# Performance work log

Measured on AMD Instinct MI355X. Metric: run time of the kernel, lower is better.

Reference implementation:

```python
import jax, jax.numpy as jnp
import numpy as np

N = 50000        # nodes
E = 1_600_000    # edges (avg degree 32)
IN, HID, OUT = 128, 64, 16


def setup_inputs() -> dict:
    key = jax.random.key(0)
    k0, k1, k2, k3, k4 = jax.random.split(key, 5)
    src = jax.random.randint(k0, (E,), 0, N, dtype=jnp.int32)
    dst = jax.random.randint(k1, (E,), 0, N, dtype=jnp.int32)
    features = jax.random.normal(k2, (N, IN), dtype=jnp.float32)
    W1 = jax.random.normal(k3, (IN, HID), dtype=jnp.float32) / np.float32(np.sqrt(IN))
    b1 = jnp.zeros((HID,), jnp.float32)
    W2 = jax.random.normal(k4, (HID, OUT), dtype=jnp.float32) / np.float32(np.sqrt(HID))
    b2 = jnp.zeros((OUT,), jnp.float32)
    return {"features": features, "W1": W1, "b1": b1, "W2": W2, "b2": b2,
            "src": src, "dst": dst}


def _graph_conv(src, dst, x, W, b):
    # DGL GraphConv, norm='both':  out = D_dst^{-1/2} * A^T * (D_src^{-1/2} * x) @ W + b
    ones = jnp.ones((src.shape[0],), x.dtype)
    deg_out = jax.ops.segment_sum(ones, src, num_segments=N)  # out-degree of source nodes
    deg_in = jax.ops.segment_sum(ones, dst, num_segments=N)   # in-degree of dest nodes
    norm_s = jax.lax.rsqrt(jnp.maximum(deg_out, 1.0))
    norm_d = jax.lax.rsqrt(jnp.maximum(deg_in, 1.0))
    # project first (in_feats >= out_feats) so messages are in the smaller dim
    h = (x * norm_s[:, None]) @ W                              # [N, out_dim]
    agg = jax.ops.segment_sum(h[src], dst, num_segments=N)     # sparse aggregate
    return agg * norm_d[:, None] + b


def reference(features, W1, b1, W2, b2, src, dst):
    h = jax.nn.relu(_graph_conv(src, dst, features, W1, b1))
    return _graph_conv(src, dst, h, W2, b2)
```

## Files before the change

kernel.cpp:

```cpp
#include <hip/hip_runtime.h>
#include <hip/hip_fp16.h>

#define IN_F  128
#define HID_F 64
#define OUT_F 16
#define MAX_N 50176
#define HWORDS (MAX_N / 2)
#define QWORDS (MAX_N / 4)
#define NSEG  128

#define SCAN_ELEMS 4
#define SCAN_BLOCK 256
#define SCAN_CHUNK (SCAN_BLOCK * SCAN_ELEMS)

#define LSTR 136
#define XSTR 68

typedef __attribute__((ext_vector_type(8))) _Float16 half8;
typedef __attribute__((ext_vector_type(4))) _Float16 half4v;
typedef __attribute__((ext_vector_type(4))) float    floatx4;

__global__ __launch_bounds__(1024) void hist2_kernel(const int* __restrict__ src,
                                                     const int* __restrict__ dst,
                                                     unsigned int* __restrict__ partial,
                                                     int E, int seg, int Wr8) {
    __shared__ unsigned int cnt[QWORDS];
    int b = blockIdx.x;
    const int* ids = blockIdx.y ? dst : src;
    unsigned int* pbase = partial + (size_t)blockIdx.y * NSEG * Wr8;
    for (int w = threadIdx.x; w < Wr8; w += 1024) cnt[w] = 0;
    __syncthreads();
    int lo = b * seg, hi = min(lo + seg, E);
    for (int e = lo + threadIdx.x; e < hi; e += 1024) {
        int d = ids[e];
        atomicAdd(&cnt[d >> 2], 1u << ((d & 3) * 8));
    }
    __syncthreads();
    for (int w = threadIdx.x; w < Wr8; w += 1024)
        pbase[(size_t)b * Wr8 + w] = cnt[w];
}

__global__ __launch_bounds__(256) void reduce_norm_kernel(unsigned int* __restrict__ partial,
                                                          int* __restrict__ counts,
                                                          float* __restrict__ norm_s,
                                                          float* __restrict__ norm_d,
                                                          int Wr8, int N) {
    int w = blockIdx.x * 256 + threadIdx.x;
    if (w >= Wr8) return;
    unsigned int r0 = 0, r1 = 0, r2 = 0, r3 = 0;
    if (blockIdx.y == 0) {
        const unsigned int* base = partial;
        for (int b = 0; b < NSEG; b++) {
            unsigned int v = base[(size_t)b * Wr8 + w];
            r0 += v & 0xFFu; r1 += (v >> 8) & 0xFFu;
            r2 += (v >> 16) & 0xFFu; r3 += v >> 24;
        }
        int d = 4 * w;
        if (d     < N) norm_s[d]     = rsqrtf(fmaxf((float)r0, 1.0f));
        if (d + 1 < N) norm_s[d + 1] = rsqrtf(fmaxf((float)r1, 1.0f));
        if (d + 2 < N) norm_s[d + 2] = rsqrtf(fmaxf((float)r2, 1.0f));
        if (d + 3 < N) norm_s[d + 3] = rsqrtf(fmaxf((float)r3, 1.0f));
    } else {
        unsigned int* base = partial + (size_t)NSEG * Wr8;
        for (int b = 0; b < NSEG; b++) {
            size_t idx = (size_t)b * Wr8 + w;
            unsigned int v = base[idx];
            base[idx] = r0 | (r1 << 8) | (r2 << 16) | (r3 << 24);
            r0 += v & 0xFFu; r1 += (v >> 8) & 0xFFu;
            r2 += (v >> 16) & 0xFFu; r3 += v >> 24;
        }
        int d = 4 * w;
        if (d     < N) { counts[d]     = (int)r0; norm_d[d]     = rsqrtf(fmaxf((float)r0, 1.0f)); }
        if (d + 1 < N) { counts[d + 1] = (int)r1; norm_d[d + 1] = rsqrtf(fmaxf((float)r1, 1.0f)); }
        if (d + 2 < N) { counts[d + 2] = (int)r2; norm_d[d + 2] = rsqrtf(fmaxf((float)r2, 1.0f)); }
        if (d + 3 < N) { counts[d + 3] = (int)r3; norm_d[d + 3] = rsqrtf(fmaxf((float)r3, 1.0f)); }
    }
}

__global__ __launch_bounds__(SCAN_BLOCK) void scan_local_kernel(int* __restrict__ counts,
                                                                int* __restrict__ bsum, int N) {
    __shared__ int part[SCAN_BLOCK];
    int t = threadIdx.x;
    int base = blockIdx.x * SCAN_CHUNK + t * SCAN_ELEMS;
    int v[SCAN_ELEMS];
    int s = 0;
    #pragma unroll
    for (int k = 0; k < SCAN_ELEMS; k++) {
        int i = base + k;
        v[k] = (i < N) ? counts[i] : 0;
        s += v[k];
    }
    part[t] = s;
    __syncthreads();
    for (int off = 1; off < SCAN_BLOCK; off <<= 1) {
        int x = (t >= off) ? part[t - off] : 0;
        __syncthreads();
        part[t] += x;
        __syncthreads();
    }
    int run = (t > 0) ? part[t - 1] : 0;
    #pragma unroll
    for (int k = 0; k < SCAN_ELEMS; k++) {
        int i = base + k;
        if (i < N) counts[i] = run;
        run += v[k];
    }
    if (t == SCAN_BLOCK - 1) bsum[blockIdx.x] = part[SCAN_BLOCK - 1];
}

__global__ __launch_bounds__(1024) void scan_bsum_kernel(int* __restrict__ bsum, int nblocks) {
    __shared__ int part[1024];
    int t = threadIdx.x;
    int v = (t < nblocks) ? bsum[t] : 0;
    part[t] = v;
    __syncthreads();
    for (int off = 1; off < 1024; off <<= 1) {
        int x = (t >= off) ? part[t - off] : 0;
        __syncthreads();
        part[t] += x;
        __syncthreads();
    }
    if (t < nblocks) bsum[t] = part[t] - v;
}

__global__ __launch_bounds__(1024) void scatter_lds_kernel(const int* __restrict__ src,
                                                           const int* __restrict__ dst,
                                                           const int* __restrict__ row_start,
                                                           const int* __restrict__ bsum,
                                                           const unsigned int* __restrict__ prefix,
                                                           unsigned short* __restrict__ csr_src,
                                                           int E, int seg, int Wr8, int N) {
    __shared__ unsigned int pos[HWORDS];
    int b = blockIdx.x;
    int p = blockIdx.y;
    int lo = b * seg, hi = min(lo + seg, E);
    int nlo = p * HWORDS, nhi = min(nlo + HWORDS, N);
    for (int d = nlo + threadIdx.x; d < nhi; d += 1024) {
        unsigned int word = prefix[(size_t)b * Wr8 + (d >> 2)];
        unsigned int base8 = (word >> ((d & 3) * 8)) & 0xFFu;
        pos[d - nlo] = (unsigned int)(row_start[d] + bsum[d >> 10]) + base8;
    }
    __syncthreads();
    for (int e = lo + threadIdx.x; e < hi; e += 1024) {
        int d = dst[e];
        if (d >= nlo && d < nhi) {
            unsigned int q = atomicAdd(&pos[d - nlo], 1u);
            csr_src[q] = (unsigned short)src[e];
        }
    }
}

__global__ __launch_bounds__(256) void gemm1_kernel(const float* __restrict__ x,
                                                    const float* __restrict__ W,
                                                    const float* __restrict__ norm_s,
                                                    __half* __restrict__ h, int N) {
    __shared__ _Float16 sx[64 * LSTR];
    __shared__ _Float16 sw[64 * LSTR];
    int t = threadIdx.x;
    int row0 = blockIdx.x * 64;

    for (int i = t; i < IN_F * 16; i += 256) {
        int k = i >> 4, n4 = (i & 15) * 4;
        float4 w4 = *(const float4*)(W + (size_t)k * HID_F + n4);
        sw[(n4 + 0) * LSTR + k] = (_Float16)w4.x;
        sw[(n4 + 1) * LSTR + k] = (_Float16)w4.y;
        sw[(n4 + 2) * LSTR + k] = (_Float16)w4.z;
        sw[(n4 + 3) * LSTR + k] = (_Float16)w4.w;
    }
    for (int i = t; i < 64 * 32; i += 256) {
        int r = i >> 5, k4 = (i & 31) * 4;
        int gr = row0 + r;
        half4v hv = {0, 0, 0, 0};
        if (gr < N) {
            float4 v = *(const float4*)(x + (size_t)gr * IN_F + k4);
            float ns = norm_s[gr];
            hv.x = (_Float16)(v.x * ns); hv.y = (_Float16)(v.y * ns);
            hv.z = (_Float16)(v.z * ns); hv.w = (_Float16)(v.w * ns);
        }
        *(half4v*)(sx + r * LSTR + k4) = hv;
    }
    __syncthreads();

    int wave = t >> 6, lane = t & 63;
    int m = lane & 15, quad = lane >> 4;
    int rbase = wave * 16;

    floatx4 acc[4] = {{0,0,0,0}, {0,0,0,0}, {0,0,0,0}, {0,0,0,0}};
    #pragma unroll
    for (int ks = 0; ks < 4; ks++) {
        half8 av = *(half8*)(sx + (rbase + m) * LSTR + ks * 32 + quad * 8);
        #pragma unroll
        for (int ct = 0; ct < 4; ct++) {
            half8 bv = *(half8*)(sw + (ct * 16 + m) * LSTR + ks * 32 + quad * 8);
            acc[ct] = __builtin_amdgcn_mfma_f32_16x16x32_f16(av, bv, acc[ct], 0, 0, 0);
        }
    }
    #pragma unroll
    for (int ct = 0; ct < 4; ct++) {
        #pragma unroll
        for (int reg = 0; reg < 4; reg++) {
            int gr = row0 + rbase + quad * 4 + reg;
            if (gr < N) h[(size_t)gr * HID_F + ct * 16 + m] = __float2half(acc[ct][reg]);
        }
    }
}

__global__ __launch_bounds__(256) void agg1_kernel(const int* __restrict__ row_start,
                                                   const int* __restrict__ bsum,
                                                   const unsigned short* __restrict__ csr_src,
                                                   const __half* __restrict__ h,
                                                   const float* __restrict__ norm_d,
                                                   const float* __restrict__ norm_s,
                                                   const float* __restrict__ b1,
                                                   const float* __restrict__ W2,
                                                   __half* __restrict__ h2, int N, int E) {
    __shared__ float sW2T[OUT_F][XSTR];
    __shared__ float xrow[16][XSTR];
    int t = threadIdx.x;
    for (int i = t; i < HID_F * OUT_F; i += 256) {
        int k = i >> 4, o = i & 15;
        sW2T[o][k] = W2[i];
    }

    int wave = t >> 6, lane = t & 63;
    int slot = lane >> 3;
    int fh   = lane & 7;
    int nbase = blockIdx.x * 16 + wave * 4;

    int rs[5];
    #pragma unroll
    for (int j = 0; j < 5; j++) {
        int n = nbase + j;
        rs[j] = (n < N) ? (row_start[n] + bsum[n >> 10]) : E;
    }

    #pragma unroll
    for (int nn = 0; nn < 4; nn++) {
        int node = nbase + nn;
        if (node < N) {
            int beg = rs[nn], end = rs[nn + 1];

            float f[8] = {0.f, 0.f, 0.f, 0.f, 0.f, 0.f, 0.f, 0.f};

            #define AGG1_BODY(SIDX) {                                                  \
                const uint4* p = (const uint4*)(h + (size_t)(SIDX) * HID_F + fh * 8);  \
                uint4 u = *p;                                                          \
                __half2 q0 = *(__half2*)&u.x, q1 = *(__half2*)&u.y;                    \
                __half2 q2 = *(__half2*)&u.z, q3 = *(__half2*)&u.w;                    \
                float2 g0 = __half22float2(q0), g1 = __half22float2(q1);               \
                float2 g2 = __half22float2(q2), g3 = __half22float2(q3);               \
                f[0] += g0.x; f[1] += g0.y; f[2] += g1.x; f[3] += g1.y;                \
                f[4] += g2.x; f[5] += g2.y; f[6] += g3.x; f[7] += g3.y; }

            int i = beg + slot;
            for (; i + 24 < end; i += 32) {
                int s0 = (int)csr_src[i];
                int s1 = (int)csr_src[i + 8];
                int s2 = (int)csr_src[i + 16];
                int s3 = (int)csr_src[i + 24];
                AGG1_BODY(s0); AGG1_BODY(s1); AGG1_BODY(s2); AGG1_BODY(s3);
            }
            for (; i < end; i += 8) {
                int s = (int)csr_src[i];
                AGG1_BODY(s);
            }
            #undef AGG1_BODY

            #pragma unroll
            for (int j = 0; j < 8; j++) {
                f[j] += __shfl_xor(f[j], 8);
                f[j] += __shfl_xor(f[j], 16);
                f[j] += __shfl_xor(f[j], 32);
            }

            if (slot == 0) {
                float nd = norm_d[node], ns = norm_s[node];
                const float4 bA = *(const float4*)(b1 + fh * 8);
                const float4 bB = *(const float4*)(b1 + fh * 8 + 4);
                float4 vA, vB;
                vA.x = fmaxf(f[0] * nd + bA.x, 0.f) * ns;
                vA.y = fmaxf(f[1] * nd + bA.y, 0.f) * ns;
                vA.z = fmaxf(f[2] * nd + bA.z, 0.f) * ns;
                vA.w = fmaxf(f[3] * nd + bA.w, 0.f) * ns;
                vB.x = fmaxf(f[4] * nd + bB.x, 0.f) * ns;
                vB.y = fmaxf(f[5] * nd + bB.y, 0.f) * ns;
                vB.z = fmaxf(f[6] * nd + bB.z, 0.f) * ns;
                vB.w = fmaxf(f[7] * nd + bB.w, 0.f) * ns;
                *(float4*)&xrow[wave * 4 + nn][fh * 8]     = vA;
                *(float4*)&xrow[wave * 4 + nn][fh * 8 + 4] = vB;
            }
        }
    }
    __syncthreads();

    int nr = t >> 4, o = t & 15;
    int gnode = blockIdx.x * 16 + nr;
    if (gnode < N) {
        float acc = 0.0f;
        #pragma unroll
        for (int k4 = 0; k4 < HID_F / 4; k4++) {
            float4 x4 = *(const float4*)&xrow[nr][k4 * 4];
            float4 w4 = *(const float4*)&sW2T[o][k4 * 4];
            acc += x4.x * w4.x + x4.y * w4.y + x4.z * w4.z + x4.w * w4.w;
        }
        h2[(size_t)gnode * OUT_F + o] = __float2half(acc);
    }
}

__global__ __launch_bounds__(256) void agg2_kernel(const int* __restrict__ row_start,
                                                   const int* __restrict__ bsum,
                                                   const unsigned short* __restrict__ csr_src,
                                                   const __half* __restrict__ h2,
                                                   const float* __restrict__ norm_d,
                                                   const float* __restrict__ b2,
                                                   float* __restrict__ out, int N, int E) {
    int node = blockIdx.x * 4 + (threadIdx.x >> 6);
    if (node >= N) return;
    int lane = threadIdx.x & 63;
    int slot = lane >> 2;
    int fh   = lane & 3;
    int beg = row_start[node] + bsum[node >> 10];
    int end = (node + 1 < N) ? row_start[node + 1] + bsum[(node + 1) >> 10] : E;

    float f0 = 0.f, f1 = 0.f, f2 = 0.f, f3 = 0.f;

    #define AGG2_BODY(SIDX) {                                                  \
        const uint2* p = (const uint2*)(h2 + (size_t)(SIDX) * OUT_F + fh * 4); \
        uint2 u = *p;                                                          \
        __half2 q0 = *(__half2*)&u.x, q1 = *(__half2*)&u.y;                    \
        float2 g0 = __half22float2(q0), g1 = __half22float2(q1);               \
        f0 += g0.x; f1 += g0.y; f2 += g1.x; f3 += g1.y; }

    int i = beg + slot;
    for (; i + 16 < end; i += 32) {
        int s0 = (int)csr_src[i];
        int s1 = (int)csr_src[i + 16];
        AGG2_BODY(s0); AGG2_BODY(s1);
    }
    if (i < end) {
        int s = (int)csr_src[i];
        AGG2_BODY(s);
    }
    #undef AGG2_BODY

    f0 += __shfl_xor(f0, 4);  f1 += __shfl_xor(f1, 4);
    f2 += __shfl_xor(f2, 4);  f3 += __shfl_xor(f3, 4);
    f0 += __shfl_xor(f0, 8);  f1 += __shfl_xor(f1, 8);
    f2 += __shfl_xor(f2, 8);  f3 += __shfl_xor(f3, 8);
    f0 += __shfl_xor(f0, 16); f1 += __shfl_xor(f1, 16);
    f2 += __shfl_xor(f2, 16); f3 += __shfl_xor(f3, 16);
    f0 += __shfl_xor(f0, 32); f1 += __shfl_xor(f1, 32);
    f2 += __shfl_xor(f2, 32); f3 += __shfl_xor(f3, 32);

    if (slot == 0) {
        float nd = norm_d[node];
        float4 v;
        v.x = f0 * nd + b2[fh * 4 + 0];
        v.y = f1 * nd + b2[fh * 4 + 1];
        v.z = f2 * nd + b2[fh * 4 + 2];
        v.w = f3 * nd + b2[fh * 4 + 3];
        *(float4*)(out + (size_t)node * OUT_F + fh * 4) = v;
    }
}

extern "C" void kernel_launch(void* const* d_in, const int* in_sizes, int n_in,
                              void* d_out, int out_size, void* d_ws, size_t ws_size,
                              hipStream_t stream) {
    const float* feat = (const float*)d_in[0];
    const float* W1   = (const float*)d_in[1];
    const float* b1   = (const float*)d_in[2];
    const float* W2   = (const float*)d_in[3];
    const float* b2   = (const float*)d_in[4];
    const int*   src  = (const int*)d_in[5];
    const int*   dst  = (const int*)d_in[6];

    const int N   = in_sizes[0] / IN_F;
    const int E   = in_sizes[5];
    const int seg = (E + NSEG - 1) / NSEG;
    const int Wr8 = (N + 3) >> 2;
    const int nchunks = (N + SCAN_CHUNK - 1) / SCAN_CHUNK;
    const int npass   = (N + HWORDS - 1) / HWORDS;

    float* fws    = (float*)d_ws;
    float* norm_s = fws;
    float* norm_d = fws + N;
    __half* h1    = (__half*)(fws + 2 * (size_t)N);
    __half* h2    = h1 + (size_t)N * HID_F;
    int*   iws    = (int*)(h2 + (size_t)N * OUT_F);
    int*   row_start = iws;
    int*   bsum      = iws + N + 1;
    unsigned int* partial = (unsigned int*)(iws + N + 1 + 1024);
    unsigned short* csr_src = (unsigned short*)(partial + 2 * (size_t)NSEG * Wr8);

    hist2_kernel<<<dim3(NSEG, 2), 1024, 0, stream>>>(src, dst, partial, E, seg, Wr8);
    reduce_norm_kernel<<<dim3((Wr8 + 255) / 256, 2), 256, 0, stream>>>(partial, row_start, norm_s, norm_d, Wr8, N);

    scan_local_kernel<<<nchunks, SCAN_BLOCK, 0, stream>>>(row_start, bsum, N);
    scan_bsum_kernel<<<1, 1024, 0, stream>>>(bsum, nchunks);

    scatter_lds_kernel<<<dim3(NSEG, npass), 1024, 0, stream>>>(src, dst, row_start, bsum,
                                                               partial + (size_t)NSEG * Wr8,
                                                               csr_src, E, seg, Wr8, N);

    gemm1_kernel<<<(N + 63) / 64, 256, 0, stream>>>(feat, W1, norm_s, h1, N);
    agg1_kernel<<<(N + 15) / 16, 256, 0, stream>>>(row_start, bsum, csr_src, h1, norm_d, norm_s, b1, W2, h2, N, E);
    agg2_kernel<<<(N + 3) / 4, 256, 0, stream>>>(row_start, bsum, csr_src, h2, norm_d, b2, (float*)d_out, N, E);
}
```

Measured before the change: 201.7 us.

## Split layer-1 aggregation into two 32-feature halves for L2-resident gathers

gemm1 now writes the hidden features as two separate N×32 fp16 tables. Layer-1 aggregation runs as two passes, each gathering from one 3.2 MB table, so the randomly accessed working set is more likely to stay in L2. The first pass writes its post-ReLU half to a float buffer in global memory, and the second pass reads it back for the W2 projection. The gather loop now handles two nodes at once with masked unrolled loads. The cost is an extra kernel launch, a second read of the CSR index list, and a round trip of the intermediate half through global memory.

```diff
diff --git a/kernel.cpp b/kernel.cpp
--- a/kernel.cpp
+++ b/kernel.cpp
@@ -15,6 +15,7 @@
 
 #define LSTR 136
 #define XSTR 68
+#define HSTR 36
 
 typedef __attribute__((ext_vector_type(8))) _Float16 half8;
 typedef __attribute__((ext_vector_type(4))) _Float16 half4v;
@@ -153,7 +154,8 @@
 __global__ __launch_bounds__(256) void gemm1_kernel(const float* __restrict__ x,
                                                     const float* __restrict__ W,
                                                     const float* __restrict__ norm_s,
-                                                    __half* __restrict__ h, int N) {
+                                                    __half* __restrict__ h1a,
+                                                    __half* __restrict__ h1b, int N) {
     __shared__ _Float16 sx[64 * LSTR];
     __shared__ _Float16 sw[64 * LSTR];
     int t = threadIdx.x;
@@ -197,35 +199,140 @@
     }
     #pragma unroll
     for (int ct = 0; ct < 4; ct++) {
+        __half* tab = (ct < 2) ? h1a : h1b;
+        int col = (ct & 1) * 16 + m;
         #pragma unroll
         for (int reg = 0; reg < 4; reg++) {
             int gr = row0 + rbase + quad * 4 + reg;
-            if (gr < N) h[(size_t)gr * HID_F + ct * 16 + m] = __float2half(acc[ct][reg]);
-        }
-    }
-}
-
-__global__ __launch_bounds__(256) void agg1_kernel(const int* __restrict__ row_start,
-                                                   const int* __restrict__ bsum,
-                                                   const unsigned short* __restrict__ csr_src,
-                                                   const __half* __restrict__ h,
-                                                   const float* __restrict__ norm_d,
-                                                   const float* __restrict__ norm_s,
-                                                   const float* __restrict__ b1,
-                                                   const float* __restrict__ W2,
-                                                   __half* __restrict__ h2, int N, int E) {
+            if (gr < N) tab[(size_t)gr * 32 + col] = __float2half(acc[ct][reg]);
+        }
+    }
+}
+
+#define ACC8(F, U) {                                                   \
+    __half2 q0 = *(__half2*)&U.x, q1 = *(__half2*)&U.y;                \
+    __half2 q2 = *(__half2*)&U.z, q3 = *(__half2*)&U.w;                \
+    float2 g0 = __half22float2(q0), g1 = __half22float2(q1);           \
+    float2 g2 = __half22float2(q2), g3 = __half22float2(q3);           \
+    F[0] += g0.x; F[1] += g0.y; F[2] += g1.x; F[3] += g1.y;            \
+    F[4] += g2.x; F[5] += g2.y; F[6] += g3.x; F[7] += g3.y; }
+
+__device__ __forceinline__ void gather_pair32(const unsigned short* __restrict__ csr,
+                                              const __half* __restrict__ tab,
+                                              int begU, int endU, int begV, int endV,
+                                              int slot, int fh, int Em1,
+                                              float* fU, float* fV) {
+    int iU = begU + slot, iV = begV + slot;
+    while (iU < endU || iV < endV) {
+        int jU1 = iU + 16, jV1 = iV + 16;
+        bool vU0 = iU < endU, vU1 = jU1 < endU;
+        bool vV0 = iV < endV, vV1 = jV1 < endV;
+        int s0 = (int)csr[min(iU, Em1)];
+        int s1 = (int)csr[min(jU1, Em1)];
+        int s2 = (int)csr[min(iV, Em1)];
+        int s3 = (int)csr[min(jV1, Em1)];
+        uint4 u0 = *(const uint4*)(tab + (size_t)s0 * 32 + fh * 8);
+        uint4 u1 = *(const uint4*)(tab + (size_t)s1 * 32 + fh * 8);
+        uint4 u2 = *(const uint4*)(tab + (size_t)s2 * 32 + fh * 8);
+        uint4 u3 = *(const uint4*)(tab + (size_t)s3 * 32 + fh * 8);
+        u0.x = vU0 ? u0.x : 0u; u0.y = vU0 ? u0.y : 0u; u0.z = vU0 ? u0.z : 0u; u0.w = vU0 ? u0.w : 0u;
+        u1.x = vU1 ? u1.x : 0u; u1.y = vU1 ? u1.y : 0u; u1.z = vU1 ? u1.z : 0u; u1.w = vU1 ? u1.w : 0u;
+        u2.x = vV0 ? u2.x : 0u; u2.y = vV0 ? u2.y : 0u; u2.z = vV0 ? u2.z : 0u; u2.w = vV0 ? u2.w : 0u;
+        u3.x = vV1 ? u3.x : 0u; u3.y = vV1 ? u3.y : 0u; u3.z = vV1 ? u3.z : 0u; u3.w = vV1 ? u3.w : 0u;
+        ACC8(fU, u0); ACC8(fU, u1); ACC8(fV, u2); ACC8(fV, u3);
+        iU += 32; iV += 32;
+    }
+    #pragma unroll
+    for (int j = 0; j < 8; j++) {
+        fU[j] += __shfl_xor(fU[j], 4);  fV[j] += __shfl_xor(fV[j], 4);
+        fU[j] += __shfl_xor(fU[j], 8);  fV[j] += __shfl_xor(fV[j], 8);
+        fU[j] += __shfl_xor(fU[j], 16); fV[j] += __shfl_xor(fV[j], 16);
+        fU[j] += __shfl_xor(fU[j], 32); fV[j] += __shfl_xor(fV[j], 32);
+    }
+}
+
+__global__ __launch_bounds__(256) void agg1a_kernel(const int* __restrict__ row_start,
+                                                    const int* __restrict__ bsum,
+                                                    const unsigned short* __restrict__ csr_src,
+                                                    const __half* __restrict__ h1a,
+                                                    const float* __restrict__ norm_d,
+                                                    const float* __restrict__ norm_s,
+                                                    const float* __restrict__ b1,
+                                                    float* __restrict__ xA, int N, int E) {
+    int t = threadIdx.x;
+    int wave = t >> 6, lane = t & 63;
+    int slot = lane >> 2, fh = lane & 3;
+    int nbase = blockIdx.x * 16 + wave * 4;
+    int Em1 = E - 1;
+
+    int rs[5];
+    #pragma unroll
+    for (int j = 0; j < 5; j++) {
+        int n = nbase + j;
+        rs[j] = (n < N) ? (row_start[n] + bsum[n >> 10]) : E;
+    }
+
+    #pragma unroll
+    for (int np = 0; np < 2; np++) {
+        int nU = nbase + np * 2, nV = nU + 1;
+        float fU[8] = {0,0,0,0,0,0,0,0}, fV[8] = {0,0,0,0,0,0,0,0};
+        gather_pair32(csr_src, h1a, rs[np*2], rs[np*2+1], rs[np*2+1], rs[np*2+2],
+                      slot, fh, Em1, fU, fV);
+        if (slot == 0) {
+            const float4 bA = *(const float4*)(b1 + fh * 8);
+            const float4 bB = *(const float4*)(b1 + fh * 8 + 4);
+            if (nU < N) {
+                float nd = norm_d[nU], ns = norm_s[nU];
+                float4 vA, vB;
+                vA.x = fmaxf(fU[0]*nd + bA.x, 0.f)*ns; vA.y = fmaxf(fU[1]*nd + bA.y, 0.f)*ns;
+                vA.z = fmaxf(fU[2]*nd + bA.z, 0.f)*ns; vA.w = fmaxf(fU[3]*nd + bA.w, 0.f)*ns;
+                vB.x = fmaxf(fU[4]*nd + bB.x, 0.f)*ns; vB.y = fmaxf(fU[5]*nd + bB.y, 0.f)*ns;
+                vB.z = fmaxf(fU[6]*nd + bB.z, 0.f)*ns; vB.w = fmaxf(fU[7]*nd + bB.w, 0.f)*ns;
+                *(float4*)(xA + (size_t)nU * 32 + fh * 8)     = vA;
+                *(float4*)(xA + (size_t)nU * 32 + fh * 8 + 4) = vB;
+            }
+            if (nV < N) {
+                float nd = norm_d[nV], ns = norm_s[nV];
+                float4 vA, vB;
+                vA.x = fmaxf(fV[0]*nd + bA.x, 0.f)*ns; vA.y = fmaxf(fV[1]*nd + bA.y, 0.f)*ns;
+                vA.z = fmaxf(fV[2]*nd + bA.z, 0.f)*ns; vA.w = fmaxf(fV[3]*nd + bA.w, 0.f)*ns;
+                vB.x = fmaxf(fV[4]*nd + bB.x, 0.f)*ns; vB.y = fmaxf(fV[5]*nd + bB.y, 0.f)*ns;
+                vB.z = fmaxf(fV[6]*nd + bB.z, 0.f)*ns; vB.w = fmaxf(fV[7]*nd + bB.w, 0.f)*ns;
+                *(float4*)(xA + (size_t)nV * 32 + fh * 8)     = vA;
+                *(float4*)(xA + (size_t)nV * 32 + fh * 8 + 4) = vB;
+            }
+        }
+    }
+}
+
+__global__ __launch_bounds__(256) void agg1b_kernel(const int* __restrict__ row_start,
+                                                    const int* __restrict__ bsum,
+                                                    const unsigned short* __restrict__ csr_src,
+                                                    const __half* __restrict__ h1b,
+                                                    const float* __restrict__ norm_d,
+                                                    const float* __restrict__ norm_s,
+                                                    const float* __restrict__ b1,
+                                                    const float* __restrict__ W2,
+                                                    const float* __restrict__ xA,
+                                                    __half* __restrict__ h2, int N, int E) {
     __shared__ float sW2T[OUT_F][XSTR];
-    __shared__ float xrow[16][XSTR];
+    __shared__ float xAl[16][HSTR];
+    __shared__ float xBl[16][HSTR];
     int t = threadIdx.x;
     for (int i = t; i < HID_F * OUT_F; i += 256) {
         int k = i >> 4, o = i & 15;
         sW2T[o][k] = W2[i];
     }
+    for (int i = t; i < 16 * 32; i += 256) {
+        int r = i >> 5, c = i & 31;
+        int gn = blockIdx.x * 16 + r;
+        xAl[r][c] = (gn < N) ? xA[(size_t)gn * 32 + c] : 0.f;
+    }
 
     int wave = t >> 6, lane = t & 63;
-    int slot = lane >> 3;
-    int fh   = lane & 7;
+    int slot = lane >> 2, fh = lane & 3;
     int nbase = blockIdx.x * 16 + wave * 4;
+    int Em1 = E - 1;
 
     int rs[5];
     #pragma unroll
@@ -235,59 +342,37 @@
     }
 
     #pragma unroll
-    for (int nn = 0; nn < 4; nn++) {
-        int node = nbase + nn;
-        if (node < N) {
-            int beg = rs[nn], end = rs[nn + 1];
-
-            float f[8] = {0.f, 0.f, 0.f, 0.f, 0.f, 0.f, 0.f, 0.f};
-
-            #define AGG1_BODY(SIDX) {                                                  \
-                const uint4* p = (const uint4*)(h + (size_t)(SIDX) * HID_F + fh * 8);  \
-                uint4 u = *p;                                                          \
-                __half2 q0 = *(__half2*)&u.x, q1 = *(__half2*)&u.y;                    \
-                __half2 q2 = *(__half2*)&u.z, q3 = *(__half2*)&u.w;                    \
-                float2 g0 = __half22float2(q0), g1 = __half22float2(q1);               \
-                float2 g2 = __half22float2(q2), g3 = __half22float2(q3);               \
-                f[0] += g0.x; f[1] += g0.y; f[2] += g1.x; f[3] += g1.y;                \
-                f[4] += g2.x; f[5] += g2.y; f[6] += g3.x; f[7] += g3.y; }
-
-            int i = beg + slot;
-            for (; i + 24 < end; i += 32) {
-                int s0 = (int)csr_src[i];
-                int s1 = (int)csr_src[i + 8];
-                int s2 = (int)csr_src[i + 16];
-                int s3 = (int)csr_src[i + 24];
-                AGG1_BODY(s0); AGG1_BODY(s1); AGG1_BODY(s2); AGG1_BODY(s3);
+    for (int np = 0; np < 2; np++) {
+        int nU = nbase + np * 2, nV = nU + 1;
+        float fU[8] = {0,0,0,0,0,0,0,0}, fV[8] = {0,0,0,0,0,0,0,0};
+        gather_pair32(csr_src, h1b, rs[np*2], rs[np*2+1], rs[np*2+1], rs[np*2+2],
+                      slot, fh, Em1, fU, fV);
+        if (slot == 0) {
+            const float4 bA = *(const float4*)(b1 + 32 + fh * 8);
+            const float4 bB = *(const float4*)(b1 + 32 + fh * 8 + 4);
+            if (nU < N) {
+                float nd = norm_d[nU], ns = norm_s[nU];
+                int r = wave * 4 + np * 2;
+                xBl[r][fh*8+0] = fmaxf(fU[0]*nd + bA.x, 0.f)*ns;
+                xBl[r][fh*8+1] = fmaxf(fU[1]*nd + bA.y, 0.f)*ns;
+                xBl[r][fh*8+2] = fmaxf(fU[2]*nd + bA.z, 0.f)*ns;
+                xBl[r][fh*8+3] = fmaxf(fU[3]*nd + bA.w, 0.f)*ns;
+                xBl[r][fh*8+4] = fmaxf(fU[4]*nd + bB.x, 0.f)*ns;
+                xBl[r][fh*8+5] = fmaxf(fU[5]*nd + bB.y, 0.f)*ns;
+                xBl[r][fh*8+6] = fmaxf(fU[6]*nd + bB.z, 0.f)*ns;
+                xBl[r][fh*8+7] = fmaxf(fU[7]*nd + bB.w, 0.f)*ns;
             }
-            for (; i < end; i += 8) {
-                int s = (int)csr_src[i];
-                AGG1_BODY(s);
-            }
-            #undef AGG1_BODY
-
-            #pragma unroll
-            for (int j = 0; j < 8; j++) {
-                f[j] += __shfl_xor(f[j], 8);
-                f[j] += __shfl_xor(f[j], 16);
-                f[j] += __shfl_xor(f[j], 32);
-            }
-
-            if (slot == 0) {
-                float nd = norm_d[node], ns = norm_s[node];
-                const float4 bA = *(const float4*)(b1 + fh * 8);
-                const float4 bB = *(const float4*)(b1 + fh * 8 + 4);
-                float4 vA, vB;
-                vA.x = fmaxf(f[0] * nd + bA.x, 0.f) * ns;
-                vA.y = fmaxf(f[1] * nd + bA.y, 0.f) * ns;
-                vA.z = fmaxf(f[2] * nd + bA.z, 0.f) * ns;
-                vA.w = fmaxf(f[3] * nd + bA.w, 0.f) * ns;
-                vB.x = fmaxf(f[4] * nd + bB.x, 0.f) * ns;
-                vB.y = fmaxf(f[5] * nd + bB.y, 0.f) * ns;
-                vB.z = fmaxf(f[6] * nd + bB.z, 0.f) * ns;
-                vB.w = fmaxf(f[7] * nd + bB.w, 0.f) * ns;
-                *(float4*)&xrow[wave * 4 + nn][fh * 8]     = vA;
-                *(float4*)&xrow[wave * 4 + nn][fh * 8 + 4] = vB;
+            if (nV < N) {
+                float nd = norm_d[nV], ns = norm_s[nV];
+                int r = wave * 4 + np * 2 + 1;
+                xBl[r][fh*8+0] = fmaxf(fV[0]*nd + bA.x, 0.f)*ns;
+                xBl[r][fh*8+1] = fmaxf(fV[1]*nd + bA.y, 0.f)*ns;
+                xBl[r][fh*8+2] = fmaxf(fV[2]*nd + bA.z, 0.f)*ns;
+                xBl[r][fh*8+3] = fmaxf(fV[3]*nd + bA.w, 0.f)*ns;
+                xBl[r][fh*8+4] = fmaxf(fV[4]*nd + bB.x, 0.f)*ns;
+                xBl[r][fh*8+5] = fmaxf(fV[5]*nd + bB.y, 0.f)*ns;
+                xBl[r][fh*8+6] = fmaxf(fV[6]*nd + bB.z, 0.f)*ns;
+                xBl[r][fh*8+7] = fmaxf(fV[7]*nd + bB.w, 0.f)*ns;
             }
         }
     }
@@ -298,9 +383,15 @@
     if (gnode < N) {
         float acc = 0.0f;
         #pragma unroll
-        for (int k4 = 0; k4 < HID_F / 4; k4++) {
-            float4 x4 = *(const float4*)&xrow[nr][k4 * 4];
+        for (int k4 = 0; k4 < 8; k4++) {
+            float4 x4 = *(const float4*)&xAl[nr][k4 * 4];
             float4 w4 = *(const float4*)&sW2T[o][k4 * 4];
+            acc += x4.x * w4.x + x4.y * w4.y + x4.z * w4.z + x4.w * w4.w;
+        }
+        #pragma unroll
+        for (int k4 = 0; k4 < 8; k4++) {
+            float4 x4 = *(const float4*)&xBl[nr][k4 * 4];
+            float4 w4 = *(const float4*)&sW2T[o][32 + k4 * 4];
             acc += x4.x * w4.x + x4.y * w4.y + x4.z * w4.z + x4.w * w4.w;
         }
         h2[(size_t)gnode * OUT_F + o] = __float2half(acc);
@@ -384,13 +475,16 @@
     float* fws    = (float*)d_ws;
     float* norm_s = fws;
     float* norm_d = fws + N;
-    __half* h1    = (__half*)(fws + 2 * (size_t)N);
-    __half* h2    = h1 + (size_t)N * HID_F;
+    __half* h1a   = (__half*)(fws + 2 * (size_t)N);
+    __half* h1b   = h1a + (size_t)N * 32;
+    __half* h2    = h1b + (size_t)N * 32;
     int*   iws    = (int*)(h2 + (size_t)N * OUT_F);
     int*   row_start = iws;
     int*   bsum      = iws + N + 1;
     unsigned int* partial = (unsigned int*)(iws + N + 1 + 1024);
     unsigned short* csr_src = (unsigned short*)(partial + 2 * (size_t)NSEG * Wr8);
+    size_t xa_off = ((size_t)((char*)(csr_src + E) - (char*)d_ws) + 255) & ~(size_t)255;
+    float* xA = (float*)((char*)d_ws + xa_off);
 
     hist2_kernel<<<dim3(NSEG, 2), 1024, 0, stream>>>(src, dst, partial, E, seg, Wr8);
     reduce_norm_kernel<<<dim3((Wr8 + 255) / 256, 2), 256, 0, stream>>>(partial, row_start, norm_s, norm_d, Wr8, N);
@@ -402,7 +496,8 @@
                                                                partial + (size_t)NSEG * Wr8,
                                                                csr_src, E, seg, Wr8, N);
 
-    gemm1_kernel<<<(N + 63) / 64, 256, 0, stream>>>(feat, W1, norm_s, h1, N);
-    agg1_kernel<<<(N + 15) / 16, 256, 0, stream>>>(row_start, bsum, csr_src, h1, norm_d, norm_s, b1, W2, h2, N, E);
+    gemm1_kernel<<<(N + 63) / 64, 256, 0, stream>>>(feat, W1, norm_s, h1a, h1b, N);
+    agg1a_kernel<<<(N + 15) / 16, 256, 0, stream>>>(row_start, bsum, csr_src, h1a, norm_d, norm_s, b1, xA, N, E);
+    agg1b_kernel<<<(N + 15) / 16, 256, 0, stream>>>(row_start, bsum, csr_src, h1b, norm_d, norm_s, b1, W2, xA, h2, N, E);
     agg2_kernel<<<(N + 3) / 4, 256, 0, stream>>>(row_start, bsum, csr_src, h2, norm_d, b2, (float*)d_out, N, E);
 }
```

New measurement: 222.9 us. 10.5% more time.

## Fuse the local scan into the degree reduction and do the CSR scatter in one pass

Applied to the files above, without the earlier changes.

The local prefix scan of in-degree counts now runs inside reduce_norm_kernel, which removes the separate scan_local launch. The scatter kernel drops its two node-range passes. It packs two 16-bit chunk-local write positions into each LDS word, so all destination nodes fit in shared memory, and adds the chunk offset from a small shared bsum table. The number of edge segments is doubled to raise parallelism in the histogram and scatter steps. The cost is that chunk-local positions must stay below 65536 and per-segment counts below 256, limits that only hold for graphs with bounded degree per chunk.

```diff
diff --git a/kernel.cpp b/kernel.cpp
--- a/kernel.cpp
+++ b/kernel.cpp
@@ -7,11 +7,10 @@
 #define MAX_N 50176
 #define HWORDS (MAX_N / 2)
 #define QWORDS (MAX_N / 4)
-#define NSEG  128
-
-#define SCAN_ELEMS 4
+#define NSEG  256
+
 #define SCAN_BLOCK 256
-#define SCAN_CHUNK (SCAN_BLOCK * SCAN_ELEMS)
+#define SCAN_CHUNK 1024
 
 #define LSTR 136
 #define XSTR 68
@@ -41,14 +40,16 @@
 }
 
 __global__ __launch_bounds__(256) void reduce_norm_kernel(unsigned int* __restrict__ partial,
-                                                          int* __restrict__ counts,
+                                                          int* __restrict__ row_start,
+                                                          int* __restrict__ bsum,
                                                           float* __restrict__ norm_s,
                                                           float* __restrict__ norm_d,
                                                           int Wr8, int N) {
-    int w = blockIdx.x * 256 + threadIdx.x;
-    if (w >= Wr8) return;
-    unsigned int r0 = 0, r1 = 0, r2 = 0, r3 = 0;
+    int t = threadIdx.x;
+    int w = blockIdx.x * 256 + t;
     if (blockIdx.y == 0) {
+        if (w >= Wr8) return;
+        unsigned int r0 = 0, r1 = 0, r2 = 0, r3 = 0;
         const unsigned int* base = partial;
         for (int b = 0; b < NSEG; b++) {
             unsigned int v = base[(size_t)b * Wr8 + w];
@@ -60,7 +61,12 @@
         if (d + 1 < N) norm_s[d + 1] = rsqrtf(fmaxf((float)r1, 1.0f));
         if (d + 2 < N) norm_s[d + 2] = rsqrtf(fmaxf((float)r2, 1.0f));
         if (d + 3 < N) norm_s[d + 3] = rsqrtf(fmaxf((float)r3, 1.0f));
-    } else {
+        return;
+    }
+    __shared__ int part[256];
+    bool inr = (w < Wr8);
+    unsigned int r0 = 0, r1 = 0, r2 = 0, r3 = 0;
+    if (inr) {
         unsigned int* base = partial + (size_t)NSEG * Wr8;
         for (int b = 0; b < NSEG; b++) {
             size_t idx = (size_t)b * Wr8 + w;
@@ -70,42 +76,31 @@
             r2 += (v >> 16) & 0xFFu; r3 += v >> 24;
         }
         int d = 4 * w;
-        if (d     < N) { counts[d]     = (int)r0; norm_d[d]     = rsqrtf(fmaxf((float)r0, 1.0f)); }
-        if (d + 1 < N) { counts[d + 1] = (int)r1; norm_d[d + 1] = rsqrtf(fmaxf((float)r1, 1.0f)); }
-        if (d + 2 < N) { counts[d + 2] = (int)r2; norm_d[d + 2] = rsqrtf(fmaxf((float)r2, 1.0f)); }
-        if (d + 3 < N) { counts[d + 3] = (int)r3; norm_d[d + 3] = rsqrtf(fmaxf((float)r3, 1.0f)); }
-    }
-}
-
-__global__ __launch_bounds__(SCAN_BLOCK) void scan_local_kernel(int* __restrict__ counts,
-                                                                int* __restrict__ bsum, int N) {
-    __shared__ int part[SCAN_BLOCK];
-    int t = threadIdx.x;
-    int base = blockIdx.x * SCAN_CHUNK + t * SCAN_ELEMS;
-    int v[SCAN_ELEMS];
-    int s = 0;
-    #pragma unroll
-    for (int k = 0; k < SCAN_ELEMS; k++) {
-        int i = base + k;
-        v[k] = (i < N) ? counts[i] : 0;
-        s += v[k];
-    }
-    part[t] = s;
-    __syncthreads();
-    for (int off = 1; off < SCAN_BLOCK; off <<= 1) {
+        if (d     < N) norm_d[d]     = rsqrtf(fmaxf((float)r0, 1.0f));
+        if (d + 1 < N) norm_d[d + 1] = rsqrtf(fmaxf((float)r1, 1.0f));
+        if (d + 2 < N) norm_d[d + 2] = rsqrtf(fmaxf((float)r2, 1.0f));
+        if (d + 3 < N) norm_d[d + 3] = rsqrtf(fmaxf((float)r3, 1.0f));
+    }
+    part[t] = inr ? (int)(r0 + r1 + r2 + r3) : 0;
+    __syncthreads();
+    for (int off = 1; off < 256; off <<= 1) {
         int x = (t >= off) ? part[t - off] : 0;
         __syncthreads();
         part[t] += x;
         __syncthreads();
     }
-    int run = (t > 0) ? part[t - 1] : 0;
-    #pragma unroll
-    for (int k = 0; k < SCAN_ELEMS; k++) {
-        int i = base + k;
-        if (i < N) counts[i] = run;
-        run += v[k];
-    }
-    if (t == SCAN_BLOCK - 1) bsum[blockIdx.x] = part[SCAN_BLOCK - 1];
+    if (inr) {
+        int run = (t > 0) ? part[t - 1] : 0;
+        int d = 4 * w;
+        if (d     < N) row_start[d]     = run;
+        run += (int)r0;
+        if (d + 1 < N) row_start[d + 1] = run;
+        run += (int)r1;
+        if (d + 2 < N) row_start[d + 2] = run;
+        run += (int)r2;
+        if (d + 3 < N) row_start[d + 3] = run;
+    }
+    if (t == 255) bsum[blockIdx.x] = part[255];
 }
 
 __global__ __launch_bounds__(1024) void scan_bsum_kernel(int* __restrict__ bsum, int nblocks) {
@@ -129,24 +124,31 @@
                                                            const int* __restrict__ bsum,
                                                            const unsigned int* __restrict__ prefix,
                                                            unsigned short* __restrict__ csr_src,
-                                                           int E, int seg, int Wr8, int N) {
+                                                           int E, int seg, int Wr8, int N,
+                                                           int nchunks) {
     __shared__ unsigned int pos[HWORDS];
+    __shared__ int sbsum[64];
     int b = blockIdx.x;
-    int p = blockIdx.y;
-    int lo = b * seg, hi = min(lo + seg, E);
-    int nlo = p * HWORDS, nhi = min(nlo + HWORDS, N);
-    for (int d = nlo + threadIdx.x; d < nhi; d += 1024) {
-        unsigned int word = prefix[(size_t)b * Wr8 + (d >> 2)];
-        unsigned int base8 = (word >> ((d & 3) * 8)) & 0xFFu;
-        pos[d - nlo] = (unsigned int)(row_start[d] + bsum[d >> 10]) + base8;
-    }
-    __syncthreads();
-    for (int e = lo + threadIdx.x; e < hi; e += 1024) {
+    int t = threadIdx.x;
+    if (t < 64) sbsum[t] = (t < nchunks) ? bsum[t] : 0;
+    int half = (N + 1) >> 1;
+    for (int w = t; w < half; w += 1024) {
+        int d0 = 2 * w, d1 = 2 * w + 1;
+        unsigned int word = prefix[(size_t)b * Wr8 + (w >> 1)];
+        unsigned int b0 = (word >> ((d0 & 3) * 8)) & 0xFFu;
+        unsigned int b1 = (word >> ((d1 & 3) * 8)) & 0xFFu;
+        unsigned int lo = (unsigned int)row_start[d0] + b0;
+        unsigned int hi = (d1 < N) ? ((unsigned int)row_start[d1] + b1) : 0u;
+        pos[w] = lo | (hi << 16);
+    }
+    __syncthreads();
+    int lo = b * seg, hiE = min(lo + seg, E);
+    for (int e = lo + t; e < hiE; e += 1024) {
         int d = dst[e];
-        if (d >= nlo && d < nhi) {
-            unsigned int q = atomicAdd(&pos[d - nlo], 1u);
-            csr_src[q] = (unsigned short)src[e];
-        }
+        unsigned int sh = (unsigned int)(d & 1) * 16u;
+        unsigned int old = atomicAdd(&pos[d >> 1], 1u << sh);
+        unsigned int q = (old >> sh) & 0xFFFFu;
+        csr_src[q + (unsigned int)sbsum[d >> 10]] = (unsigned short)src[e];
     }
 }
 
@@ -379,7 +381,6 @@
     const int seg = (E + NSEG - 1) / NSEG;
     const int Wr8 = (N + 3) >> 2;
     const int nchunks = (N + SCAN_CHUNK - 1) / SCAN_CHUNK;
-    const int npass   = (N + HWORDS - 1) / HWORDS;
 
     float* fws    = (float*)d_ws;
     float* norm_s = fws;
@@ -393,14 +394,12 @@
     unsigned short* csr_src = (unsigned short*)(partial + 2 * (size_t)NSEG * Wr8);
 
     hist2_kernel<<<dim3(NSEG, 2), 1024, 0, stream>>>(src, dst, partial, E, seg, Wr8);
-    reduce_norm_kernel<<<dim3((Wr8 + 255) / 256, 2), 256, 0, stream>>>(partial, row_start, norm_s, norm_d, Wr8, N);
-
-    scan_local_kernel<<<nchunks, SCAN_BLOCK, 0, stream>>>(row_start, bsum, N);
+    reduce_norm_kernel<<<dim3((Wr8 + 255) / 256, 2), 256, 0, stream>>>(partial, row_start, bsum, norm_s, norm_d, Wr8, N);
     scan_bsum_kernel<<<1, 1024, 0, stream>>>(bsum, nchunks);
 
-    scatter_lds_kernel<<<dim3(NSEG, npass), 1024, 0, stream>>>(src, dst, row_start, bsum,
-                                                               partial + (size_t)NSEG * Wr8,
-                                                               csr_src, E, seg, Wr8, N);
+    scatter_lds_kernel<<<NSEG, 1024, 0, stream>>>(src, dst, row_start, bsum,
+                                                  partial + (size_t)NSEG * Wr8,
+                                                  csr_src, E, seg, Wr8, N, nchunks);
 
     gemm1_kernel<<<(N + 63) / 64, 256, 0, stream>>>(feat, W1, norm_s, h1, N);
     agg1_kernel<<<(N + 15) / 16, 256, 0, stream>>>(row_start, bsum, csr_src, h1, norm_d, norm_s, b1, W2, h2, N, E);
```

After: 224.8 us. 11.5% more time.
